# Performance work log

Hardware: AMD Instinct MI355X
Metric: run time of the kernel (lower is better)

## Reference

```python
import jax, jax.numpy as jnp
import numpy as np

NEG_SLOPE = 0.2


def gat_layer(x, src, dst, W, a_src, a_dst, b, heads, ch, concat, n_nodes):
    # x: [N, F_in], W: [F_in, heads*ch]
    h = (x @ W).reshape(n_nodes, heads, ch)              # [N, H, C]
    alpha_src = jnp.sum(h * a_src, axis=-1)              # [N, H]
    alpha_dst = jnp.sum(h * a_dst, axis=-1)              # [N, H]
    e = jax.nn.leaky_relu(alpha_src[src] + alpha_dst[dst], NEG_SLOPE)  # [E, H]
    # segment softmax over edges grouped by destination node
    e_max = jax.ops.segment_max(e, dst, num_segments=n_nodes)          # [N, H]
    ex = jnp.exp(e - e_max[dst])                                       # [E, H]
    denom = jax.ops.segment_sum(ex, dst, num_segments=n_nodes)         # [N, H]
    alpha = ex / denom[dst]                                            # [E, H]
    msg = h[src] * alpha[:, :, None]                                   # [E, H, C]
    out = jax.ops.segment_sum(msg, dst, num_segments=n_nodes)          # [N, H, C]
    if concat:
        out = out.reshape(n_nodes, heads * ch)
    else:
        out = out.mean(axis=1)
    return out + b


def setup_inputs() -> dict:
    key = jax.random.key(0)
    ks = jax.random.split(key, 16)
    N, E, F_in = 50000, 800000, 128
    H, C, OUT = 4, 32, 64
    x = jax.random.normal(ks[0], (N, F_in), dtype=jnp.float32)
    edge_index = jax.random.randint(ks[1], (2, E), 0, N, dtype=jnp.int64)
    s = 0.1
    return {
        "x": x,
        "edge_index": edge_index,
        "W1": jax.random.normal(ks[2], (F_in, H * C), dtype=jnp.float32) * s,
        "a_src1": jax.random.normal(ks[3], (H, C), dtype=jnp.float32) * s,
        "a_dst1": jax.random.normal(ks[4], (H, C), dtype=jnp.float32) * s,
        "b1": jnp.zeros((H * C,), dtype=jnp.float32),
        "W2": jax.random.normal(ks[5], (H * C, H * C), dtype=jnp.float32) * s,
        "a_src2": jax.random.normal(ks[6], (H, C), dtype=jnp.float32) * s,
        "a_dst2": jax.random.normal(ks[7], (H, C), dtype=jnp.float32) * s,
        "b2": jnp.zeros((H * C,), dtype=jnp.float32),
        "W3": jax.random.normal(ks[8], (H * C, H * OUT), dtype=jnp.float32) * s,
        "a_src3": jax.random.normal(ks[9], (H, OUT), dtype=jnp.float32) * s,
        "a_dst3": jax.random.normal(ks[10], (H, OUT), dtype=jnp.float32) * s,
        "b3": jnp.zeros((OUT,), dtype=jnp.float32),
    }


def reference(x, edge_index, W1, a_src1, a_dst1, b1, W2, a_src2, a_dst2, b2,
              W3, a_src3, a_dst3, b3):
    N = x.shape[0]
    # PyG GATConv default add_self_loops=True
    loop = jnp.arange(N, dtype=edge_index.dtype)
    src = jnp.concatenate([edge_index[0], loop])
    dst = jnp.concatenate([edge_index[1], loop])
    h = gat_layer(x, src, dst, W1, a_src1, a_dst1, b1, 4, 32, True, N)
    h = gat_layer(h, src, dst, W2, a_src2, a_dst2, b2, 4, 32, True, N)
    out = gat_layer(h, src, dst, W3, a_src3, a_dst3, b3, 4, 64, False, N)
    return out
```

## Files before the change

kernel.cpp:

```cpp
#include <hip/hip_runtime.h>
#include <hip/hip_fp16.h>

constexpr int HEADS = 4;

typedef _Float16 half8 __attribute__((ext_vector_type(8)));
typedef _Float16 half2v __attribute__((ext_vector_type(2)));
typedef float f32x4 __attribute__((ext_vector_type(4)));

__device__ __forceinline__ float lrelu(float x) { return x > 0.f ? x : 0.2f * x; }


__global__ void count_deg_kernel(const int* __restrict__ ei, int* __restrict__ deg,
                                 int E, int N) {
  int e = blockIdx.x * 256 + threadIdx.x;
  int EP = E + N;
  if (e < EP) {
    int d = (e < E) ? ei[E + e] : (e - E);
    atomicAdd(&deg[d], 1);
  }
}

__global__ void scan_block_kernel(const int* __restrict__ deg, int* __restrict__ rowp,
                                  int* __restrict__ partials, int N) {
  __shared__ int sm[1024];
  int t = threadIdx.x;
  int i = blockIdx.x * 1024 + t;
  int v = (i < N) ? deg[i] : 0;
  sm[t] = v;
  __syncthreads();
  for (int off = 1; off < 1024; off <<= 1) {
    int tmp = (t >= off) ? sm[t - off] : 0;
    __syncthreads();
    sm[t] += tmp;
    __syncthreads();
  }
  if (i < N) rowp[i] = sm[t] - v;
  if (t == 1023) partials[blockIdx.x] = sm[t];
}

__global__ void scan_partials_kernel(int* partials, int nb) {
  __shared__ int sm[1024];
  int t = threadIdx.x;
  int v = (t < nb) ? partials[t] : 0;
  sm[t] = v;
  __syncthreads();
  for (int off = 1; off < 1024; off <<= 1) {
    int tmp = (t >= off) ? sm[t - off] : 0;
    __syncthreads();
    sm[t] += tmp;
    __syncthreads();
  }
  if (t < nb) partials[t] = sm[t] - v;
}

__global__ void add_off_kernel(int* __restrict__ rowp, const int* __restrict__ partials,
                               int N, int EP) {
  int i = blockIdx.x * 256 + threadIdx.x;
  if (i < N) rowp[i] += partials[i >> 10];
  if (i == 0) rowp[N] = EP;
}

__global__ void scatter_kernel(const int* __restrict__ ei, const int* __restrict__ rowp,
                               int* __restrict__ cursor, int* __restrict__ col,
                               int E, int N) {
  int e = blockIdx.x * 256 + threadIdx.x;
  int EP = E + N;
  if (e < EP) {
    int s, d;
    if (e < E) { s = ei[e]; d = ei[E + e]; }
    else       { s = e - E; d = e - E; }
    int pos = rowp[d] + atomicAdd(&cursor[d], 1);
    col[pos] = s;
  }
}


__global__ void convert_wt3_kernel(const float* __restrict__ W1, _Float16* __restrict__ Wt1,
                                   const float* __restrict__ W2, _Float16* __restrict__ Wt2,
                                   const float* __restrict__ W3, _Float16* __restrict__ Wt3) {
  const float* W; _Float16* Wt; int Fout;
  if (blockIdx.y == 0)      { W = W1; Wt = Wt1; Fout = 128; }
  else if (blockIdx.y == 1) { W = W2; Wt = Wt2; Fout = 128; }
  else                      { W = W3; Wt = Wt3; Fout = 256; }
  int i = blockIdx.x * 256 + threadIdx.x;
  if (i < 128 * Fout) {
    int c = i >> 7, k = i & 127;
    Wt[c * 128 + k] = (_Float16)W[k * Fout + c];
  }
}


template <int AF32, int CPH>
__global__ __launch_bounds__(256) void gemm_mfma_kernel(
    const void* __restrict__ Xv, const _Float16* __restrict__ Wt,
    const float* __restrict__ a_s, const float* __restrict__ a_d,
    _Float16* __restrict__ O, float* __restrict__ asrc, float* __restrict__ adst,
    int N, int Fout) {
  __shared__ __align__(16) char Bl[32768];
  const int t = threadIdx.x;
  const int w = t >> 6;
  const int lane = t & 63;
  const int r = lane & 15, g = lane >> 4;
  const int row0 = blockIdx.x * 64 + w * 16;
  const int colpan = blockIdx.y * 128;

#pragma unroll
  for (int i = 0; i < 8; ++i) {
    int lin = i * 256 + t;
    int c0 = lin >> 4;
    int kb = lin & 15;
    half8 v = *(const half8*)&Wt[(size_t)(colpan + c0) * 128 + kb * 8];
    int addr = (c0 * 256 + kb * 16) ^ ((c0 & 7) << 4);
    *(half8*)(Bl + addr) = v;
  }
  __syncthreads();

  int rowl = row0 + r;
  if (rowl >= N) rowl = N - 1;

  f32x4 acc[8];
#pragma unroll
  for (int c = 0; c < 8; ++c) acc[c] = {0.f, 0.f, 0.f, 0.f};

#pragma unroll
  for (int s = 0; s < 4; ++s) {
    half8 a;
    if constexpr (AF32) {
      const float* X = (const float*)Xv;
      float4 a0 = *(const float4*)&X[(size_t)rowl * 128 + s * 32 + g * 8];
      float4 a1 = *(const float4*)&X[(size_t)rowl * 128 + s * 32 + g * 8 + 4];
      a = half8{(_Float16)a0.x, (_Float16)a0.y, (_Float16)a0.z, (_Float16)a0.w,
                (_Float16)a1.x, (_Float16)a1.y, (_Float16)a1.z, (_Float16)a1.w};
    } else {
      const _Float16* X = (const _Float16*)Xv;
      a = *(const half8*)&X[(size_t)rowl * 128 + s * 32 + g * 8];
    }
#pragma unroll
    for (int c = 0; c < 8; ++c) {
      int colr = c * 16 + r;
      int addr = (colr * 256 + s * 64 + g * 16) ^ ((colr & 7) << 4);
      half8 b = *(const half8*)(Bl + addr);
      acc[c] = __builtin_amdgcn_mfma_f32_16x16x32_f16(a, b, acc[c], 0, 0, 0);
    }
  }

#pragma unroll
  for (int c = 0; c < 8; ++c) {
    int ocol = colpan + c * 16 + r;
#pragma unroll
    for (int q = 0; q < 4; ++q) {
      int orow = row0 + g * 4 + q;
      if (orow < N) O[(size_t)orow * Fout + ocol] = (_Float16)acc[c][q];
    }
  }

  constexpr int HPP = 8 / CPH;
  constexpr int C = CPH * 16;
  const int hbase = blockIdx.y * HPP;
  float ps[4][HPP], pd[4][HPP];
#pragma unroll
  for (int q = 0; q < 4; ++q)
#pragma unroll
    for (int hh = 0; hh < HPP; ++hh) { ps[q][hh] = 0.f; pd[q][hh] = 0.f; }

#pragma unroll
  for (int c = 0; c < 8; ++c) {
    int hh = c / CPH;
    int ch = (c % CPH) * 16 + r;
    float asv = a_s[(hbase + hh) * C + ch];
    float adv = a_d[(hbase + hh) * C + ch];
#pragma unroll
    for (int q = 0; q < 4; ++q) {
      ps[q][hh] += acc[c][q] * asv;
      pd[q][hh] += acc[c][q] * adv;
    }
  }
#pragma unroll
  for (int m = 1; m < 16; m <<= 1) {
#pragma unroll
    for (int q = 0; q < 4; ++q)
#pragma unroll
      for (int hh = 0; hh < HPP; ++hh) {
        ps[q][hh] += __shfl_xor(ps[q][hh], m, 64);
        pd[q][hh] += __shfl_xor(pd[q][hh], m, 64);
      }
  }
  if (r == 0) {
#pragma unroll
    for (int q = 0; q < 4; ++q) {
      int row = row0 + g * 4 + q;
      if (row < N) {
#pragma unroll
        for (int hh = 0; hh < HPP; ++hh) {
          asrc[row * 4 + hbase + hh] = ps[q][hh];
          adst[row * 4 + hbase + hh] = pd[q][hh];
        }
      }
    }
  }
}


__global__ __launch_bounds__(256) void aggregate_concat_kernel(
    const _Float16* __restrict__ H, const float* __restrict__ asrc,
    const float* __restrict__ adst, const float* __restrict__ bias,
    const int* __restrict__ rowp, const int* __restrict__ col,
    _Float16* __restrict__ out, int N) {
  int n = blockIdx.x * 4 + (threadIdx.x >> 6);
  if (n >= N) return;
  int lane = threadIdx.x & 63;
  int h = lane >> 4;
  float ad = adst[n * 4 + h];
  int j = rowp[n], end = rowp[n + 1];
  const bool comp = (lane & 15) < 8;
  const int bsrc = lane & 48;
  float ax = 0.f, ay = 0.f, denom = 0.f;
  for (; j + 7 < end; j += 8) {
    float wpre = 0.f;
    if (comp) {
      int sc = col[j + (lane & 7)];
      wpre = __expf(lrelu(asrc[sc * 4 + h] + ad));
    }
    int s[8]; half2v f[8]; float wk[8];
#pragma unroll
    for (int k = 0; k < 8; ++k) s[k] = col[j + k];
#pragma unroll
    for (int k = 0; k < 8; ++k) {
      wk[k] = __shfl(wpre, bsrc | k, 64);
      f[k] = *(const half2v*)&H[(size_t)s[k] * 128 + lane * 2];
    }
#pragma unroll
    for (int k = 0; k < 8; ++k) {
      denom += wk[k];
      ax += wk[k] * (float)f[k].x;
      ay += wk[k] * (float)f[k].y;
    }
  }
  for (; j < end; ++j) {
    int s0 = col[j];
    float w0 = __expf(lrelu(asrc[s0 * 4 + h] + ad));
    half2v f0 = *(const half2v*)&H[(size_t)s0 * 128 + lane * 2];
    denom += w0;
    ax += w0 * (float)f0.x;
    ay += w0 * (float)f0.y;
  }
  float inv = 1.f / denom;
  half2v o;
  o.x = (_Float16)(ax * inv + bias[lane * 2]);
  o.y = (_Float16)(ay * inv + bias[lane * 2 + 1]);
  *(half2v*)&out[(size_t)n * 128 + lane * 2] = o;
}


__global__ __launch_bounds__(128) void aggregate_mean_kernel(
    const _Float16* __restrict__ H, const float* __restrict__ asrc,
    const float* __restrict__ adst, const float* __restrict__ bias,
    const int* __restrict__ rowp, const int* __restrict__ col,
    float* __restrict__ out, int N) {
  __shared__ float2 red[128];
  int n = blockIdx.x;
  int t = threadIdx.x;
  int h = t >> 5;
  int lane = t & 63;
  float ad = adst[n * 4 + h];
  int j = rowp[n], end = rowp[n + 1];
  const bool comp = (lane & 31) < 8;
  const int bsrc = lane & 32;
  float ax = 0.f, ay = 0.f, denom = 0.f;
  for (; j + 7 < end; j += 8) {
    float wpre = 0.f;
    if (comp) {
      int sc = col[j + (lane & 7)];
      wpre = __expf(lrelu(asrc[sc * 4 + h] + ad));
    }
    int s[8]; half2v f[8]; float wk[8];
#pragma unroll
    for (int k = 0; k < 8; ++k) s[k] = col[j + k];
#pragma unroll
    for (int k = 0; k < 8; ++k) {
      wk[k] = __shfl(wpre, bsrc | k, 64);
      f[k] = *(const half2v*)&H[(size_t)s[k] * 256 + t * 2];
    }
#pragma unroll
    for (int k = 0; k < 8; ++k) {
      denom += wk[k];
      ax += wk[k] * (float)f[k].x;
      ay += wk[k] * (float)f[k].y;
    }
  }
  for (; j < end; ++j) {
    int s0 = col[j];
    float w0 = __expf(lrelu(asrc[s0 * 4 + h] + ad));
    half2v f0 = *(const half2v*)&H[(size_t)s0 * 256 + t * 2];
    denom += w0;
    ax += w0 * (float)f0.x;
    ay += w0 * (float)f0.y;
  }
  float inv = 1.f / denom;
  red[t] = make_float2(ax * inv, ay * inv);
  __syncthreads();
  if (t < 32) {
    float2 r0 = red[t], r1 = red[t + 32], r2 = red[t + 64], r3 = red[t + 96];
    float2 o = make_float2(0.25f * (r0.x + r1.x + r2.x + r3.x) + bias[t * 2],
                           0.25f * (r0.y + r1.y + r2.y + r3.y) + bias[t * 2 + 1]);
    *(float2*)&out[n * 64 + t * 2] = o;
  }
}


extern "C" void kernel_launch(void* const* d_in, const int* in_sizes, int n_in,
                              void* d_out, int out_size, void* d_ws, size_t ws_size,
                              hipStream_t stream) {
  const float* x   = (const float*)d_in[0];
  const int*   ei  = (const int*)d_in[1];
  const float* W1  = (const float*)d_in[2];
  const float* as1 = (const float*)d_in[3];
  const float* ad1 = (const float*)d_in[4];
  const float* b1  = (const float*)d_in[5];
  const float* W2  = (const float*)d_in[6];
  const float* as2 = (const float*)d_in[7];
  const float* ad2 = (const float*)d_in[8];
  const float* b2  = (const float*)d_in[9];
  const float* W3  = (const float*)d_in[10];
  const float* as3 = (const float*)d_in[11];
  const float* ad3 = (const float*)d_in[12];
  const float* b3  = (const float*)d_in[13];
  float* out = (float*)d_out;

  const int N  = in_sizes[0] / 128;
  const int E  = in_sizes[1] / 2;
  const int EP = E + N;

  char* p = (char*)d_ws;
  auto carve = [&](size_t bytes) -> void* {
    void* r = (void*)p;
    p += (bytes + 255) & ~size_t(255);
    return r;
  };
  int*      deg  = (int*)carve(size_t(N) * 4);
  int*      rowp = (int*)carve(size_t(N + 1) * 4);
  int*      cur  = (int*)carve(size_t(N) * 4);
  int*      part = (int*)carve(1024 * 4);
  int*      col  = (int*)carve(size_t(EP) * 4);
  float*    asrc = (float*)carve(size_t(N) * HEADS * 4);
  float*    adst = (float*)carve(size_t(N) * HEADS * 4);
  _Float16* Wt1  = (_Float16*)carve(128 * 128 * 2);
  _Float16* Wt2  = (_Float16*)carve(128 * 128 * 2);
  _Float16* Wt3  = (_Float16*)carve(256 * 128 * 2);
  _Float16* Hb   = (_Float16*)carve(size_t(N) * 256 * 2);
  _Float16* Ab   = (_Float16*)carve(size_t(N) * 128 * 2);

  hipMemsetAsync(deg, 0, size_t(N) * 4, stream);
  hipMemsetAsync(cur, 0, size_t(N) * 4, stream);

  int gEP = (EP + 255) / 256;
  count_deg_kernel<<<gEP, 256, 0, stream>>>(ei, deg, E, N);
  int nb = (N + 1023) / 1024;
  scan_block_kernel<<<nb, 1024, 0, stream>>>(deg, rowp, part, N);
  scan_partials_kernel<<<1, 1024, 0, stream>>>(part, nb);
  add_off_kernel<<<(N + 256) / 256, 256, 0, stream>>>(rowp, part, N, EP);
  scatter_kernel<<<gEP, 256, 0, stream>>>(ei, rowp, cur, col, E, N);

  convert_wt3_kernel<<<dim3(128, 3), 256, 0, stream>>>(W1, Wt1, W2, Wt2, W3, Wt3);

  int gM = (N + 63) / 64;
  int gN4 = (N + 3) / 4;

  gemm_mfma_kernel<1, 2><<<dim3(gM, 1), 256, 0, stream>>>(
      x, Wt1, as1, ad1, Hb, asrc, adst, N, 128);
  aggregate_concat_kernel<<<gN4, 256, 0, stream>>>(Hb, asrc, adst, b1, rowp, col, Ab, N);
  gemm_mfma_kernel<0, 2><<<dim3(gM, 1), 256, 0, stream>>>(
      Ab, Wt2, as2, ad2, Hb, asrc, adst, N, 128);
  aggregate_concat_kernel<<<gN4, 256, 0, stream>>>(Hb, asrc, adst, b2, rowp, col, Ab, N);
  gemm_mfma_kernel<0, 4><<<dim3(gM, 2), 256, 0, stream>>>(
      Ab, Wt3, as3, ad3, Hb, asrc, adst, N, 256);
  aggregate_mean_kernel<<<N, 128, 0, stream>>>(Hb, asrc, adst, b3, rowp, col, out, N);
}
```

Measured before the change: 406.2 us.

## Split edges across lane groups with 16-byte feature loads in aggregation kernels

Both aggregation kernels now give each lane an 8-wide half8 slice of a feature row. Each wave handles several edges at once, one per lane group, and the partial sums are reduced across groups with xor shuffles. The attention-weight shuffle broadcast and the shared-memory head reduction are gone: each lane computes its own edge weight, and the mean kernel reduces heads with shuffles while packing two nodes per block. The aim is wider, more vectorised gathers and more edges in flight per wave, paid for with redundant exp computation and extra cross-lane reductions.

```diff
diff --git a/kernel.cpp b/kernel.cpp
--- a/kernel.cpp
+++ b/kernel.cpp
@@ -4,7 +4,6 @@
 constexpr int HEADS = 4;
 
 typedef _Float16 half8 __attribute__((ext_vector_type(8)));
-typedef _Float16 half2v __attribute__((ext_vector_type(2)));
 typedef float f32x4 __attribute__((ext_vector_type(4)));
 
 __device__ __forceinline__ float lrelu(float x) { return x > 0.f ? x : 0.2f * x; }
@@ -209,46 +208,52 @@
   int n = blockIdx.x * 4 + (threadIdx.x >> 6);
   if (n >= N) return;
   int lane = threadIdx.x & 63;
-  int h = lane >> 4;
+  int g = lane >> 4;
+  int l16 = lane & 15;
+  int h = l16 >> 2;
   float ad = adst[n * 4 + h];
   int j = rowp[n], end = rowp[n + 1];
-  const bool comp = (lane & 15) < 8;
-  const int bsrc = lane & 48;
-  float ax = 0.f, ay = 0.f, denom = 0.f;
-  for (; j + 7 < end; j += 8) {
-    float wpre = 0.f;
-    if (comp) {
-      int sc = col[j + (lane & 7)];
-      wpre = __expf(lrelu(asrc[sc * 4 + h] + ad));
-    }
-    int s[8]; half2v f[8]; float wk[8];
-#pragma unroll
-    for (int k = 0; k < 8; ++k) s[k] = col[j + k];
-#pragma unroll
-    for (int k = 0; k < 8; ++k) {
-      wk[k] = __shfl(wpre, bsrc | k, 64);
-      f[k] = *(const half2v*)&H[(size_t)s[k] * 128 + lane * 2];
-    }
-#pragma unroll
-    for (int k = 0; k < 8; ++k) {
-      denom += wk[k];
-      ax += wk[k] * (float)f[k].x;
-      ay += wk[k] * (float)f[k].y;
-    }
-  }
-  for (; j < end; ++j) {
-    int s0 = col[j];
+  float acc[8] = {};
+  float denom = 0.f;
+  for (; j + 8 <= end; j += 8) {
+    int s0 = col[j + g];
+    int s1 = col[j + 4 + g];
     float w0 = __expf(lrelu(asrc[s0 * 4 + h] + ad));
-    half2v f0 = *(const half2v*)&H[(size_t)s0 * 128 + lane * 2];
-    denom += w0;
-    ax += w0 * (float)f0.x;
-    ay += w0 * (float)f0.y;
-  }
-  float inv = 1.f / denom;
-  half2v o;
-  o.x = (_Float16)(ax * inv + bias[lane * 2]);
-  o.y = (_Float16)(ay * inv + bias[lane * 2 + 1]);
-  *(half2v*)&out[(size_t)n * 128 + lane * 2] = o;
+    float w1 = __expf(lrelu(asrc[s1 * 4 + h] + ad));
+    half8 f0 = *(const half8*)&H[(size_t)s0 * 128 + l16 * 8];
+    half8 f1 = *(const half8*)&H[(size_t)s1 * 128 + l16 * 8];
+    denom += w0 + w1;
+#pragma unroll
+    for (int c = 0; c < 8; ++c) acc[c] += w0 * (float)f0[c] + w1 * (float)f1[c];
+  }
+  for (int base = j; base < end; base += 4) {
+    int idx = base + g;
+    if (idx < end) {
+      int s0 = col[idx];
+      float w0 = __expf(lrelu(asrc[s0 * 4 + h] + ad));
+      half8 f0 = *(const half8*)&H[(size_t)s0 * 128 + l16 * 8];
+      denom += w0;
+#pragma unroll
+      for (int c = 0; c < 8; ++c) acc[c] += w0 * (float)f0[c];
+    }
+  }
+#pragma unroll
+  for (int m = 16; m <= 32; m <<= 1) {
+    denom += __shfl_xor(denom, m, 64);
+#pragma unroll
+    for (int c = 0; c < 8; ++c) acc[c] += __shfl_xor(acc[c], m, 64);
+  }
+  if (g == 0) {
+    float inv = 1.f / denom;
+    float4 b0 = *(const float4*)&bias[l16 * 8];
+    float4 b1 = *(const float4*)&bias[l16 * 8 + 4];
+    half8 o;
+    o[0] = (_Float16)(acc[0] * inv + b0.x); o[1] = (_Float16)(acc[1] * inv + b0.y);
+    o[2] = (_Float16)(acc[2] * inv + b0.z); o[3] = (_Float16)(acc[3] * inv + b0.w);
+    o[4] = (_Float16)(acc[4] * inv + b1.x); o[5] = (_Float16)(acc[5] * inv + b1.y);
+    o[6] = (_Float16)(acc[6] * inv + b1.z); o[7] = (_Float16)(acc[7] * inv + b1.w);
+    *(half8*)&out[(size_t)n * 128 + l16 * 8] = o;
+  }
 }
 
 
@@ -257,53 +262,57 @@
     const float* __restrict__ adst, const float* __restrict__ bias,
     const int* __restrict__ rowp, const int* __restrict__ col,
     float* __restrict__ out, int N) {
-  __shared__ float2 red[128];
-  int n = blockIdx.x;
-  int t = threadIdx.x;
-  int h = t >> 5;
-  int lane = t & 63;
+  int n = blockIdx.x * 2 + (threadIdx.x >> 6);
+  if (n >= N) return;
+  int lane = threadIdx.x & 63;
+  int g = lane >> 5;
+  int l32 = lane & 31;
+  int h = l32 >> 3;
   float ad = adst[n * 4 + h];
   int j = rowp[n], end = rowp[n + 1];
-  const bool comp = (lane & 31) < 8;
-  const int bsrc = lane & 32;
-  float ax = 0.f, ay = 0.f, denom = 0.f;
-  for (; j + 7 < end; j += 8) {
-    float wpre = 0.f;
-    if (comp) {
-      int sc = col[j + (lane & 7)];
-      wpre = __expf(lrelu(asrc[sc * 4 + h] + ad));
-    }
-    int s[8]; half2v f[8]; float wk[8];
-#pragma unroll
-    for (int k = 0; k < 8; ++k) s[k] = col[j + k];
-#pragma unroll
-    for (int k = 0; k < 8; ++k) {
-      wk[k] = __shfl(wpre, bsrc | k, 64);
-      f[k] = *(const half2v*)&H[(size_t)s[k] * 256 + t * 2];
-    }
-#pragma unroll
-    for (int k = 0; k < 8; ++k) {
-      denom += wk[k];
-      ax += wk[k] * (float)f[k].x;
-      ay += wk[k] * (float)f[k].y;
-    }
-  }
-  for (; j < end; ++j) {
-    int s0 = col[j];
+  float acc[8] = {};
+  float denom = 0.f;
+  for (; j + 4 <= end; j += 4) {
+    int s0 = col[j + g];
+    int s1 = col[j + 2 + g];
     float w0 = __expf(lrelu(asrc[s0 * 4 + h] + ad));
-    half2v f0 = *(const half2v*)&H[(size_t)s0 * 256 + t * 2];
-    denom += w0;
-    ax += w0 * (float)f0.x;
-    ay += w0 * (float)f0.y;
-  }
-  float inv = 1.f / denom;
-  red[t] = make_float2(ax * inv, ay * inv);
-  __syncthreads();
-  if (t < 32) {
-    float2 r0 = red[t], r1 = red[t + 32], r2 = red[t + 64], r3 = red[t + 96];
-    float2 o = make_float2(0.25f * (r0.x + r1.x + r2.x + r3.x) + bias[t * 2],
-                           0.25f * (r0.y + r1.y + r2.y + r3.y) + bias[t * 2 + 1]);
-    *(float2*)&out[n * 64 + t * 2] = o;
+    float w1 = __expf(lrelu(asrc[s1 * 4 + h] + ad));
+    half8 f0 = *(const half8*)&H[(size_t)s0 * 256 + l32 * 8];
+    half8 f1 = *(const half8*)&H[(size_t)s1 * 256 + l32 * 8];
+    denom += w0 + w1;
+#pragma unroll
+    for (int c = 0; c < 8; ++c) acc[c] += w0 * (float)f0[c] + w1 * (float)f1[c];
+  }
+  for (int base = j; base < end; base += 2) {
+    int idx = base + g;
+    if (idx < end) {
+      int s0 = col[idx];
+      float w0 = __expf(lrelu(asrc[s0 * 4 + h] + ad));
+      half8 f0 = *(const half8*)&H[(size_t)s0 * 256 + l32 * 8];
+      denom += w0;
+#pragma unroll
+      for (int c = 0; c < 8; ++c) acc[c] += w0 * (float)f0[c];
+    }
+  }
+  denom += __shfl_xor(denom, 32, 64);
+#pragma unroll
+  for (int c = 0; c < 8; ++c) acc[c] += __shfl_xor(acc[c], 32, 64);
+  float inv = 0.25f / denom;
+#pragma unroll
+  for (int c = 0; c < 8; ++c) acc[c] *= inv;
+#pragma unroll
+  for (int m = 8; m <= 16; m <<= 1) {
+#pragma unroll
+    for (int c = 0; c < 8; ++c) acc[c] += __shfl_xor(acc[c], m, 64);
+  }
+  if (lane < 8) {
+    int cb = lane * 8;
+    float4 b0 = *(const float4*)&bias[cb];
+    float4 b1 = *(const float4*)&bias[cb + 4];
+    float4 o0 = make_float4(acc[0] + b0.x, acc[1] + b0.y, acc[2] + b0.z, acc[3] + b0.w);
+    float4 o1 = make_float4(acc[4] + b1.x, acc[5] + b1.y, acc[6] + b1.z, acc[7] + b1.w);
+    *(float4*)&out[(size_t)n * 64 + cb] = o0;
+    *(float4*)&out[(size_t)n * 64 + cb + 4] = o1;
   }
 }
 
@@ -365,6 +374,7 @@
 
   int gM = (N + 63) / 64;
   int gN4 = (N + 3) / 4;
+  int gN2 = (N + 1) / 2;
 
   gemm_mfma_kernel<1, 2><<<dim3(gM, 1), 256, 0, stream>>>(
       x, Wt1, as1, ad1, Hb, asrc, adst, N, 128);
@@ -374,5 +384,5 @@
   aggregate_concat_kernel<<<gN4, 256, 0, stream>>>(Hb, asrc, adst, b2, rowp, col, Ab, N);
   gemm_mfma_kernel<0, 4><<<dim3(gM, 2), 256, 0, stream>>>(
       Ab, Wt3, as3, ad3, Hb, asrc, adst, N, 256);
-  aggregate_mean_kernel<<<N, 128, 0, stream>>>(Hb, asrc, adst, b3, rowp, col, out, N);
-}
+  aggregate_mean_kernel<<<gN2, 128, 0, stream>>>(Hb, asrc, adst, b3, rowp, col, out, N);
+}
```

Result: faster. 361.9 us (-10.9%).
